# Kernel tuning notes

Hardware: AMD Instinct MI355X
Metric: run time of the kernel (lower is better)

## Reference

```python
import jax, jax.numpy as jnp
import numpy as np


def _gru_cell(x, h, W_ih, W_hh, b_ih, b_hh):
    # torch.nn.GRUCell math. x: [T,H], h: [T,H]; W_*: [3H,H]; b_*: [3H]
    gi = x @ W_ih.T + b_ih          # [T,3H]
    gh = h @ W_hh.T + b_hh          # [T,3H]
    i_r, i_z, i_n = jnp.split(gi, 3, axis=-1)
    h_r, h_z, h_n = jnp.split(gh, 3, axis=-1)
    r = jax.nn.sigmoid(i_r + h_r)
    z = jax.nn.sigmoid(i_z + h_z)
    n = jnp.tanh(i_n + r * h_n)
    return (1.0 - z) * n + z * h


def setup_inputs() -> dict:
    key = jax.random.key(0)
    ks = jax.random.split(key, 7)
    S, T, H = 65536, 8192, 1024
    bound = 1.0 / np.sqrt(H)  # torch GRUCell init scale
    return {
        "speaker_memory": jax.random.normal(ks[0], (S, H), dtype=jnp.float32),
        "speaker_ids": jax.random.randint(ks[1], (T,), 0, S, dtype=jnp.int32),
        "edu_reps": jax.random.normal(ks[2], (T, H), dtype=jnp.float32),
        "W_ih": jax.random.uniform(ks[3], (3 * H, H), jnp.float32, -bound, bound),
        "W_hh": jax.random.uniform(ks[4], (3 * H, H), jnp.float32, -bound, bound),
        "b_ih": jax.random.uniform(ks[5], (3 * H,), jnp.float32, -bound, bound),
        "b_hh": jax.random.uniform(ks[6], (3 * H,), jnp.float32, -bound, bound),
    }


def reference(speaker_memory, speaker_ids, edu_reps, W_ih, W_hh, b_ih, b_hh):
    # The torch loop reads h from the ORIGINAL speaker_memory for every step,
    # so all T GRU updates are independent; for duplicate speaker ids the last
    S, H = speaker_memory.shape
    T = speaker_ids.shape[0]
    h = speaker_memory[speaker_ids]                      # [T,H] gather
    new_h = _gru_cell(edu_reps, h, W_ih, W_hh, b_ih, b_hh)  # [T,H]
    # last occurrence position of each speaker id (int min for untouched ids)
    last_pos = jax.ops.segment_max(jnp.arange(T), speaker_ids, num_segments=S)
    touched = last_pos >= 0                              # [S]
    gathered = new_h[jnp.clip(last_pos, 0, T - 1)]       # [S,H]
    return jnp.where(touched[:, None], gathered, speaker_memory)
```

## Files before the change

### kernel.cpp

```cpp
#include <hip/hip_runtime.h>
#include <hip/hip_bf16.h>
#include <stdint.h>
#include <stddef.h>

typedef short short8 __attribute__((ext_vector_type(8)));
typedef float f32x4 __attribute__((ext_vector_type(4)));

#define SROWS 65536
#define TROWS 8192
#define HDIM  1024
#define KDIM  2048
#define NDIM  4096
#define NT    (KDIM / 64)

__device__ __forceinline__ unsigned short f2bf(float f) {
  union { float f; uint32_t u; } v; v.f = f;
  uint32_t u = v.u;
  uint32_t r = (u + 0x7FFFu + ((u >> 16) & 1u)) >> 16;
  return (unsigned short)r;
}

__device__ __forceinline__ float fast_sigmoid(float x) {
  return __builtin_amdgcn_rcpf(1.0f + __builtin_amdgcn_exp2f(-1.44269504f * x));
}
__device__ __forceinline__ float fast_tanh(float x) {
  return 1.0f - 2.0f * __builtin_amdgcn_rcpf(1.0f + __builtin_amdgcn_exp2f(2.88539008f * x));
}


__global__ __launch_bounds__(256) void k_initlp(int* lp) {
  int i = blockIdx.x * 256 + threadIdx.x;
  if (i < SROWS) lp[i] = -1;
}

__global__ __launch_bounds__(256) void k_lp(const int* __restrict__ sid, int* lp) {
  int i = blockIdx.x * 256 + threadIdx.x;
  if (i < TROWS) atomicMax(&lp[sid[i]], i);
}

__global__ __launch_bounds__(256) void k_flags(const int* __restrict__ lp,
                                               unsigned long long* __restrict__ flagb) {
  int i = blockIdx.x * 256 + threadIdx.x;
  unsigned long long m = __ballot(lp[i] < 0);
  if ((threadIdx.x & 63) == 0) flagb[i >> 6] = m;
}

__global__ __launch_bounds__(256) void k_bias(const float* __restrict__ bih,
                                              const float* __restrict__ bhh,
                                              float* __restrict__ btab) {
  int j = blockIdx.x * 256 + threadIdx.x;
  if (j < HDIM) {
    btab[4*j+0] = bih[j] + bhh[j];
    btab[4*j+1] = bih[j+HDIM] + bhh[j+HDIM];
    btab[4*j+2] = bih[j+2*HDIM];
    btab[4*j+3] = bhh[j+2*HDIM];
  }
}

__global__ __launch_bounds__(256) void k_build_A(const float* __restrict__ edu,
                                                 const float* __restrict__ mem,
                                                 const int* __restrict__ sid,
                                                 unsigned short* __restrict__ Ac) {
  const int idx = blockIdx.x * 256 + threadIdx.x;
  const int t  = idx >> 8;
  const int k0 = (idx & 255) << 3;
  const float* src;
  if (k0 < HDIM) src = edu + (size_t)t * HDIM + k0;
  else           src = mem + (size_t)sid[t] * HDIM + (k0 - HDIM);
  f32x4 f0 = *(const f32x4*)src;
  f32x4 f1 = *(const f32x4*)(src + 4);
  short8 v;
  v[0]=(short)f2bf(f0[0]); v[1]=(short)f2bf(f0[1]); v[2]=(short)f2bf(f0[2]); v[3]=(short)f2bf(f0[3]);
  v[4]=(short)f2bf(f1[0]); v[5]=(short)f2bf(f1[1]); v[6]=(short)f2bf(f1[2]); v[7]=(short)f2bf(f1[3]);
  *(short8*)(Ac + (size_t)idx * 8) = v;
}

__global__ __launch_bounds__(256) void k_build_B(const float* __restrict__ Wih,
                                                 const float* __restrict__ Whh,
                                                 unsigned short* __restrict__ Bc) {
  const int idx = blockIdx.x * 256 + threadIdx.x;
  const int c  = idx >> 8;
  const int k0 = (idx & 255) << 3;
  const int j  = c >> 2;
  const int g  = c & 3;
  const float* src = nullptr;
  if (g == 0)      src = (k0 < HDIM) ? Wih + (size_t)j * HDIM + k0
                                     : Whh + (size_t)j * HDIM + (k0 - HDIM);
  else if (g == 1) src = (k0 < HDIM) ? Wih + (size_t)(j + HDIM) * HDIM + k0
                                     : Whh + (size_t)(j + HDIM) * HDIM + (k0 - HDIM);
  else if (g == 2) { if (k0 < HDIM)  src = Wih + (size_t)(j + 2*HDIM) * HDIM + k0; }
  else             { if (k0 >= HDIM) src = Whh + (size_t)(j + 2*HDIM) * HDIM + (k0 - HDIM); }
  short8 v = (short8)0;
  if (src) {
    f32x4 f0 = *(const f32x4*)src;
    f32x4 f1 = *(const f32x4*)(src + 4);
    v[0]=(short)f2bf(f0[0]); v[1]=(short)f2bf(f0[1]); v[2]=(short)f2bf(f0[2]); v[3]=(short)f2bf(f0[3]);
    v[4]=(short)f2bf(f1[0]); v[5]=(short)f2bf(f1[1]); v[6]=(short)f2bf(f1[2]); v[7]=(short)f2bf(f1[3]);
  }
  *(short8*)(Bc + (size_t)idx * 8) = v;
}


#define FENCE() asm volatile("" ::: "memory")
#define BAR()   __builtin_amdgcn_s_barrier()
#define LGKM0() asm volatile("s_waitcnt lgkmcnt(0)" ::: "memory")
#define VM(N)   asm volatile("s_waitcnt vmcnt(" #N ")" ::: "memory")

#define STAGE(p0, p1, ldsoff)                                                              \
  __builtin_amdgcn_global_load_lds((const __attribute__((address_space(1))) void*)(p0),   \
      (__attribute__((address_space(3))) void*)(smem + (ldsoff) + w * 1024), 16, 0, 0);    \
  __builtin_amdgcn_global_load_lds((const __attribute__((address_space(1))) void*)(p1),   \
      (__attribute__((address_space(3))) void*)(smem + (ldsoff) + 8192 + w * 1024), 16, 0, 0);

#define LDF(base, frag, koff) (*(const short8*)(smem + (base) + (size_t)(frag) * 2048 + (koff)))

__global__ __launch_bounds__(512, 2)
void k_gru8(const unsigned short* __restrict__ Ac,
            const unsigned short* __restrict__ Bc,
            const float* __restrict__ mem,
            const int* __restrict__ sid,
            const int* __restrict__ lp,
            const unsigned long long* __restrict__ flagb,
            const float* __restrict__ btab,
            float* __restrict__ out) {
  extern __shared__ char smem[];

  const int tid  = threadIdx.x;
  const int lane = tid & 63;
  const int w    = tid >> 6;
  const int wm   = w >> 2;
  const int wn   = w & 3;
  const int l15  = lane & 15;
  const int l4   = lane >> 4;

  const int bid = blockIdx.x;
  const int swz = (bid & 7) * 64 + (bid >> 3);
  const int t0  = (swz >> 4) * 256;
  const int c0  = (swz & 15) * 256;

  const int srow0 = tid >> 3;
  const int srow1 = 64 + srow0;
  const int scol  = ((tid & 7) * 8) ^ (((tid >> 3) & 7) << 3);

  const unsigned short* pA0r0 = Ac + (size_t)(t0 +       srow0) * KDIM + scol;
  const unsigned short* pA0r1 = Ac + (size_t)(t0 +       srow1) * KDIM + scol;
  const unsigned short* pA1r0 = Ac + (size_t)(t0 + 128 + srow0) * KDIM + scol;
  const unsigned short* pA1r1 = Ac + (size_t)(t0 + 128 + srow1) * KDIM + scol;
  const unsigned short* pB0r0 = Bc + (size_t)(c0 +       srow0) * KDIM + scol;
  const unsigned short* pB0r1 = Bc + (size_t)(c0 +       srow1) * KDIM + scol;
  const unsigned short* pB1r0 = Bc + (size_t)(c0 + 128 + srow0) * KDIM + scol;
  const unsigned short* pB1r1 = Bc + (size_t)(c0 + 128 + srow1) * KDIM + scol;

  const int rsw = (l15 & 7) << 4;
  const size_t foff0 = (size_t)l15 * 128 + ((l4 * 16)      ^ rsw);
  const size_t foff1 = (size_t)l15 * 128 + ((64 + l4 * 16) ^ rsw);

  f32x4 acc[8][4];
#pragma unroll
  for (int i = 0; i < 8; i++)
#pragma unroll
    for (int j = 0; j < 4; j++) acc[i][j] = (f32x4){0.f, 0.f, 0.f, 0.f};

  const int cbase = bid << 7;
  const unsigned long long fw0 = flagb[bid * 2];
  const unsigned long long fw1 = flagb[bid * 2 + 1];
  const int ccp  = tid >> 8;
  const int ccol = (tid & 255) << 2;
  f32x4 cp0, cp1;
  bool  cv0 = false, cv1 = false;
  int   cs0 = 0, cs1 = 0;

  STAGE(pA0r0, pA0r1, 0);
  STAGE(pA1r0, pA1r1, 16384);
  STAGE(pB0r0, pB0r1, 32768);
  STAGE(pB1r0, pB1r1, 49152);
  STAGE(pB0r0 + 64, pB0r1 + 64, 65536 + 32768);
  STAGE(pB1r0 + 64, pB1r1 + 64, 65536 + 49152);
  VM(4);
  FENCE(); BAR();

  for (int t = 0; t < NT; ++t) {
    const int cur = t & 1, nxt = cur ^ 1;
    const size_t abase = (size_t)cur * 65536 + (size_t)wm * 16384;
    const size_t bbase = (size_t)cur * 65536 + 32768 + (size_t)(wn >> 1) * 16384
                       + (size_t)(wn & 1) * 8192;
    const int kt1 = (t + 1 < NT) ? t + 1 : NT - 1;
    const int kt2 = (t + 2 < NT) ? t + 2 : NT - 1;

    short8 bf[4][2];
#pragma unroll
    for (int q = 0; q < 4; q++) {
      const int m0 = 2 * q;
      if (q == 0) {
#pragma unroll
        for (int n = 0; n < 4; n++) {
          bf[n][0] = LDF(bbase, n, foff0);
          bf[n][1] = LDF(bbase, n, foff1);
        }
      }
      short8 af[2][2];
      af[0][0] = LDF(abase, m0,     foff0);
      af[0][1] = LDF(abase, m0,     foff1);
      af[1][0] = LDF(abase, m0 + 1, foff0);
      af[1][1] = LDF(abase, m0 + 1, foff1);

      if (q == 0)      { STAGE(pA0r0 + kt1 * 64, pA0r1 + kt1 * 64, (size_t)nxt * 65536); }
      else if (q == 1) { STAGE(pA1r0 + kt1 * 64, pA1r1 + kt1 * 64, (size_t)nxt * 65536 + 16384); }
      else if (q == 2) { STAGE(pB0r0 + kt2 * 64, pB0r1 + kt2 * 64, (size_t)cur * 65536 + 32768); }
      else             { STAGE(pB1r0 + kt2 * 64, pB1r1 + kt2 * 64, (size_t)cur * 65536 + 49152); }

      FENCE(); BAR();
      LGKM0();
      __builtin_amdgcn_s_setprio(1);
#pragma unroll
      for (int i = 0; i < 2; i++)
#pragma unroll
        for (int n = 0; n < 4; n++) {
          acc[m0 + i][n] = __builtin_amdgcn_mfma_f32_16x16x32_bf16(af[i][0], bf[n][0], acc[m0 + i][n], 0, 0, 0);
          acc[m0 + i][n] = __builtin_amdgcn_mfma_f32_16x16x32_bf16(af[i][1], bf[n][1], acc[m0 + i][n], 0, 0, 0);
        }
      __builtin_amdgcn_s_setprio(0);
      if (q == 3) {
        VM(4);
        if (cv0) __builtin_nontemporal_store(cp0, (f32x4*)&out[(size_t)cs0 * HDIM + ccol]);
        if (cv1) __builtin_nontemporal_store(cp1, (f32x4*)&out[(size_t)cs1 * HDIM + ccol]);
        {
          const int rr0 = 4 * t + ccp, rr1 = rr0 + 2;
          const unsigned long long fwt = (t < 16) ? fw0 : fw1;
          cv0 = (fwt >> (rr0 & 63)) & 1ull;
          cv1 = (fwt >> (rr1 & 63)) & 1ull;
          cs0 = cbase + rr0; cs1 = cbase + rr1;
          if (cv0) cp0 = __builtin_nontemporal_load((const f32x4*)&mem[(size_t)cs0 * HDIM + ccol]);
          if (cv1) cp1 = __builtin_nontemporal_load((const f32x4*)&mem[(size_t)cs1 * HDIM + ccol]);
        }
      }
      FENCE(); BAR();
    }
  }

  VM(0);
  if (cv0) __builtin_nontemporal_store(cp0, (f32x4*)&out[(size_t)cs0 * HDIM + ccol]);
  if (cv1) __builtin_nontemporal_store(cp1, (f32x4*)&out[(size_t)cs1 * HDIM + ccol]);
  __syncthreads();
  float* epi = (float*)smem;
  const int jfirst = ((c0 + wn * 64) >> 2) + l4 * 4;

#pragma unroll
  for (int mf = 0; mf < 8; mf++) {
#pragma unroll
    for (int nf = 0; nf < 4; nf++)
#pragma unroll
      for (int r = 0; r < 4; r++)
        epi[w * 1088 + (l4 * 4 + r) * 68 + nf * 16 + l15] = acc[mf][nf][r];
    __syncthreads();

    const int trow = t0 + wm * 128 + mf * 16 + l15;
    const int s    = sid[trow];
    const bool wr  = (lp[s] == trow);

    f32x4 q[4];
#pragma unroll
    for (int jj = 0; jj < 4; jj++)
      q[jj] = *(const f32x4*)&epi[w * 1088 + l15 * 68 + l4 * 16 + jj * 4];

    f32x4 hv = *(const f32x4*)&mem[(size_t)s * HDIM + jfirst];
    f32x4 o;
#pragma unroll
    for (int jj = 0; jj < 4; jj++) {
      const int j = jfirst + jj;
      f32x4 bt = *(const f32x4*)&btab[4 * j];
      float rr = fast_sigmoid(q[jj][0] + bt[0]);
      float zz = fast_sigmoid(q[jj][1] + bt[1]);
      float nn = fast_tanh(q[jj][2] + bt[2] + rr * (q[jj][3] + bt[3]));
      o[jj] = (1.0f - zz) * nn + zz * hv[jj];
    }
    if (wr) __builtin_nontemporal_store(o, (f32x4*)&out[(size_t)s * HDIM + jfirst]);
    __syncthreads();
  }
}


extern "C" void kernel_launch(void* const* d_in, const int* in_sizes, int n_in,
                              void* d_out, int out_size, void* d_ws, size_t ws_size,
                              hipStream_t stream) {
  const float* mem = (const float*)d_in[0];
  const int*   sid = (const int*)d_in[1];
  const float* edu = (const float*)d_in[2];
  const float* Wih = (const float*)d_in[3];
  const float* Whh = (const float*)d_in[4];
  const float* bih = (const float*)d_in[5];
  const float* bhh = (const float*)d_in[6];
  float* out = (float*)d_out;

  char* p = (char*)d_ws;
  unsigned short* Ac = (unsigned short*)p; p += (size_t)TROWS * KDIM * 2;
  unsigned short* Bc = (unsigned short*)p; p += (size_t)NDIM * KDIM * 2;
  int*   lp   = (int*)p;   p += (size_t)SROWS * 4;
  float* btab = (float*)p; p += (size_t)HDIM * 4 * 4;
  unsigned long long* flagb = (unsigned long long*)p; p += (size_t)(SROWS / 64) * 8;

  hipFuncSetAttribute((const void*)k_gru8, hipFuncAttributeMaxDynamicSharedMemorySize, 131072);

  hipLaunchKernelGGL(k_initlp, dim3(SROWS / 256), dim3(256), 0, stream, lp);
  hipLaunchKernelGGL(k_lp, dim3(TROWS / 256), dim3(256), 0, stream, sid, lp);
  hipLaunchKernelGGL(k_flags, dim3(SROWS / 256), dim3(256), 0, stream, lp, flagb);
  hipLaunchKernelGGL(k_bias, dim3(4), dim3(256), 0, stream, bih, bhh, btab);
  hipLaunchKernelGGL(k_build_A, dim3((TROWS * KDIM / 8) / 256), dim3(256), 0, stream, edu, mem, sid, Ac);
  hipLaunchKernelGGL(k_build_B, dim3((NDIM * KDIM / 8) / 256), dim3(256), 0, stream, Wih, Whh, Bc);
  hipLaunchKernelGGL(k_gru8, dim3(512), dim3(512), 131072, stream,
                     Ac, Bc, mem, sid, lp, flagb, btab, out);
}
```

Measured before the change: 246.9 us.

## Warp-specialize untouched-row copy into dedicated producer waves in fused GEMM kernel

Adds four extra waves per block (768 threads) that copy untouched speaker_memory rows to the output. Previously the compute waves interleaved that copy inside the MFMA k-loop. The copy waves issue matching barrier counts so they stay in lockstep with the compute waves, which removes the extra global traffic and vmcnt waits from the GEMM path. In exchange the launch bounds tighten to (768,3), which may sharply cut the register budget for the 128-float accumulator and cause spills. The hand-counted barrier matching is also fragile.

```diff
diff --git a/kernel.cpp b/kernel.cpp
--- a/kernel.cpp
+++ b/kernel.cpp
@@ -114,26 +114,51 @@
 
 #define LDF(base, frag, koff) (*(const short8*)(smem + (base) + (size_t)(frag) * 2048 + (koff)))
 
-__global__ __launch_bounds__(512, 2)
-void k_gru8(const unsigned short* __restrict__ Ac,
-            const unsigned short* __restrict__ Bc,
-            const float* __restrict__ mem,
-            const int* __restrict__ sid,
-            const int* __restrict__ lp,
-            const unsigned long long* __restrict__ flagb,
-            const float* __restrict__ btab,
-            float* __restrict__ out) {
+__global__ __launch_bounds__(768, 3)
+void k_fused(const unsigned short* __restrict__ Ac,
+             const unsigned short* __restrict__ Bc,
+             const float* __restrict__ mem,
+             const int* __restrict__ sid,
+             const int* __restrict__ lp,
+             const unsigned long long* __restrict__ flagb,
+             const float* __restrict__ btab,
+             float* __restrict__ out) {
   extern __shared__ char smem[];
-
-  const int tid  = threadIdx.x;
+  const int tid = threadIdx.x;
+  const int bid = blockIdx.x;
+  const int w   = tid >> 6;
+
+  if (w >= 8) {
+    const int ct    = tid - 512;
+    const int col   = ct << 2;
+    const int rbase = bid << 7;
+    const unsigned long long f0 = flagb[bid * 2];
+    const unsigned long long f1 = flagb[bid * 2 + 1];
+
+    bool pv = (f0 & 1ull) != 0;
+    f32x4 d = {0.f, 0.f, 0.f, 0.f};
+    if (pv) d = __builtin_nontemporal_load((const f32x4*)&mem[(size_t)rbase * HDIM + col]);
+    for (int r = 1; r < 128; ++r) {
+      const unsigned long long fw = (r < 64) ? f0 : f1;
+      const bool v = (fw >> (r & 63)) & 1ull;
+      f32x4 nd = {0.f, 0.f, 0.f, 0.f};
+      if (v)  nd = __builtin_nontemporal_load((const f32x4*)&mem[(size_t)(rbase + r) * HDIM + col]);
+      if (pv) __builtin_nontemporal_store(d, (f32x4*)&out[(size_t)(rbase + r - 1) * HDIM + col]);
+      pv = v; d = nd;
+      BAR(); BAR();
+    }
+    if (pv) __builtin_nontemporal_store(d, (f32x4*)&out[(size_t)(rbase + 127) * HDIM + col]);
+    BAR(); BAR();
+    for (int i = 0; i < 18; ++i) BAR();
+    return;
+  }
+
   const int lane = tid & 63;
-  const int w    = tid >> 6;
   const int wm   = w >> 2;
   const int wn   = w & 3;
   const int l15  = lane & 15;
   const int l4   = lane >> 4;
 
-  const int bid = blockIdx.x;
   const int swz = (bid & 7) * 64 + (bid >> 3);
   const int t0  = (swz >> 4) * 256;
   const int c0  = (swz & 15) * 256;
@@ -160,15 +185,6 @@
   for (int i = 0; i < 8; i++)
 #pragma unroll
     for (int j = 0; j < 4; j++) acc[i][j] = (f32x4){0.f, 0.f, 0.f, 0.f};
-
-  const int cbase = bid << 7;
-  const unsigned long long fw0 = flagb[bid * 2];
-  const unsigned long long fw1 = flagb[bid * 2 + 1];
-  const int ccp  = tid >> 8;
-  const int ccol = (tid & 255) << 2;
-  f32x4 cp0, cp1;
-  bool  cv0 = false, cv1 = false;
-  int   cs0 = 0, cs1 = 0;
 
   STAGE(pA0r0, pA0r1, 0);
   STAGE(pA1r0, pA1r1, 16384);
@@ -220,27 +236,12 @@
           acc[m0 + i][n] = __builtin_amdgcn_mfma_f32_16x16x32_bf16(af[i][1], bf[n][1], acc[m0 + i][n], 0, 0, 0);
         }
       __builtin_amdgcn_s_setprio(0);
-      if (q == 3) {
-        VM(4);
-        if (cv0) __builtin_nontemporal_store(cp0, (f32x4*)&out[(size_t)cs0 * HDIM + ccol]);
-        if (cv1) __builtin_nontemporal_store(cp1, (f32x4*)&out[(size_t)cs1 * HDIM + ccol]);
-        {
-          const int rr0 = 4 * t + ccp, rr1 = rr0 + 2;
-          const unsigned long long fwt = (t < 16) ? fw0 : fw1;
-          cv0 = (fwt >> (rr0 & 63)) & 1ull;
-          cv1 = (fwt >> (rr1 & 63)) & 1ull;
-          cs0 = cbase + rr0; cs1 = cbase + rr1;
-          if (cv0) cp0 = __builtin_nontemporal_load((const f32x4*)&mem[(size_t)cs0 * HDIM + ccol]);
-          if (cv1) cp1 = __builtin_nontemporal_load((const f32x4*)&mem[(size_t)cs1 * HDIM + ccol]);
-        }
-      }
+      if (q == 3) { VM(4); }
       FENCE(); BAR();
     }
   }
 
   VM(0);
-  if (cv0) __builtin_nontemporal_store(cp0, (f32x4*)&out[(size_t)cs0 * HDIM + ccol]);
-  if (cv1) __builtin_nontemporal_store(cp1, (f32x4*)&out[(size_t)cs1 * HDIM + ccol]);
   __syncthreads();
   float* epi = (float*)smem;
   const int jfirst = ((c0 + wn * 64) >> 2) + l4 * 4;
@@ -299,7 +300,7 @@
   float* btab = (float*)p; p += (size_t)HDIM * 4 * 4;
   unsigned long long* flagb = (unsigned long long*)p; p += (size_t)(SROWS / 64) * 8;
 
-  hipFuncSetAttribute((const void*)k_gru8, hipFuncAttributeMaxDynamicSharedMemorySize, 131072);
+  hipFuncSetAttribute((const void*)k_fused, hipFuncAttributeMaxDynamicSharedMemorySize, 131072);
 
   hipLaunchKernelGGL(k_initlp, dim3(SROWS / 256), dim3(256), 0, stream, lp);
   hipLaunchKernelGGL(k_lp, dim3(TROWS / 256), dim3(256), 0, stream, sid, lp);
@@ -307,6 +308,6 @@
   hipLaunchKernelGGL(k_bias, dim3(4), dim3(256), 0, stream, bih, bhh, btab);
   hipLaunchKernelGGL(k_build_A, dim3((TROWS * KDIM / 8) / 256), dim3(256), 0, stream, edu, mem, sid, Ac);
   hipLaunchKernelGGL(k_build_B, dim3((NDIM * KDIM / 8) / 256), dim3(256), 0, stream, Wih, Whh, Bc);
-  hipLaunchKernelGGL(k_gru8, dim3(512), dim3(512), 131072, stream,
+  hipLaunchKernelGGL(k_fused, dim3(512), dim3(768), 131072, stream,
                      Ac, Bc, mem, sid, lp, flagb, btab, out);
 }
```

Result: slower. 659.2 us (+167.0%).
